# Kernel tuning notes

Hardware: AMD Instinct MI355X
Metric: run time of the kernel (lower is better)

Reference implementation:

```python
import jax, jax.numpy as jnp
import numpy as np
from jax import lax

B, R, C = 4, 64, 192          # batch, input_resolution, dim
WN, K = 16, 3                 # ka_win_num, kernel_size
WS = R // 4                   # window_size = R / sqrt(WN) = 16
DN = ('NCHW', 'OIHW', 'NCHW')


def setup_inputs() -> dict:
    key = jax.random.key(0)
    ks = jax.random.split(key, 12)
    rn = lambda k, shp, s=0.05: jax.random.normal(k, shp, dtype=jnp.float32) * s
    return {
        'x': jax.random.normal(ks[0], (B, R * R, C), dtype=jnp.float32),
        'conv1_w': rn(ks[1], (WN * C, 1, K, K), 0.1),
        'dc_w': rn(ks[2], (WN, C)),                             # grouped 1x1 (WN*C -> WN)
        'dc_b': jnp.zeros((WN,), jnp.float32),
        'l1_w': rn(ks[3], (4 * WN, WN)),
        'l1_b': jnp.zeros((4 * WN,), jnp.float32),
        'l2_w': rn(ks[4], (WN, 4 * WN)),
        'l2_b': jnp.zeros((WN,), jnp.float32),
        'gk_w': rn(ks[5], (WN,)),                               # 1x1 conv WN -> 1
        'gk_b': jnp.zeros((1,), jnp.float32),
        'fusion_w': rn(ks[6], (C, (WN + 1) * C)),               # 1x1 conv (WN+1)*C -> C
        'fusion_b': jnp.zeros((C,), jnp.float32),
    }


def _forward(x, conv1_w, dc_w, dc_b, l1_w, l1_b, l2_w, l2_b, gk_w, gk_b,
             fusion_w, fusion_b):
    # pad_feature_map is a no-op since R % WS == 0.
    xw = x.reshape(B, R // WS, WS, R // WS, WS, C)
    xw = xw.transpose(0, 1, 3, 5, 2, 4).reshape(B, WN * C, WS, WS)

    # convlayer1: depthwise conv over all WN*C channels
    y = lax.conv_general_dilated(xw, conv1_w, (1, 1), [(1, 1), (1, 1)],
                                 dimension_numbers=DN,
                                 feature_group_count=WN * C)  # (B, WN*C, WS, WS)

    # WinKernel_Reweight: pool -> grouped 1x1 -> gelu -> 1x1 -> sigmoid
    pooled = y.mean(axis=(2, 3)).reshape(B, WN, C)
    w = jnp.einsum('bwc,wc->bw', pooled, dc_w) + dc_b          # downchannel (groups=WN)
    w = jax.nn.gelu(w @ l1_w.T + l1_b, approximate=False)      # (B, 4*WN)
    w = jax.nn.sigmoid(w @ l2_w.T + l2_b)                      # (B, WN)

    kern = conv1_w.reshape(WN, C, K, K)
    kern = w[:, :, None, None, None] * kern[None]              # (B, WN, C, K, K)

    # global kernel: 1x1 conv across the WN axis
    gk = jnp.einsum('bwcij,w->bcij', kern, gk_w) + gk_b[0]     # (B, C, K, K)
    all_k = jnp.concatenate([kern, gk[:, None]], axis=1)       # (B, WN+1, C, K, K)

    # dynamic depthwise conv on the full map, per sample
    xf = x.reshape(B, R, R, C).transpose(0, 3, 1, 2)           # (B, C, R, R)
    xrep = jnp.tile(xf, (1, WN + 1, 1, 1))                     # (B, (WN+1)*C, R, R)
    kflat = all_k.reshape(B, (WN + 1) * C, 1, K, K)

    def dw(xi, ki):  # xi: ((WN+1)*C, R, R), ki: ((WN+1)*C, 1, K, K)
        return lax.conv_general_dilated(xi[None], ki, (1, 1), [(1, 1), (1, 1)],
                                        dimension_numbers=DN,
                                        feature_group_count=(WN + 1) * C)[0]

    out = jax.vmap(dw)(xrep, kflat)                            # (B, (WN+1)*C, R, R)

    # fusion 1x1 conv -> (B, C, R, R) -> (B, L, C)
    out = jnp.einsum('bdhw,cd->bhwc', out, fusion_w) + fusion_b
    return out.reshape(B, R * R, C)


def reference(x, conv1_w, dc_w, dc_b, l1_w, l1_b, l2_w, l2_b, gk_w, gk_b,
              fusion_w, fusion_b):
    return _forward(x, conv1_w, dc_w, dc_b, l1_w, l1_b, l2_w, l2_b,
                    gk_w, gk_b, fusion_w, fusion_b)
```

## Files before the change

### kernel.cpp

```cpp
#include <hip/hip_runtime.h>
#include <hip/hip_bf16.h>
#include <math.h>

#define B_  4
#define R_  64
#define C_  192
#define WN_ 16


typedef __attribute__((ext_vector_type(8))) short short8;
typedef __attribute__((ext_vector_type(4))) float floatx4;

static __device__ __forceinline__ unsigned short f2bf(float f) {
    union { float f; unsigned u; } v; v.f = f;
    unsigned r = v.u + 0x7fffu + ((v.u >> 16) & 1u);
    return (unsigned short)(r >> 16);
}

__global__ __launch_bounds__(256) void pre_kernel(
        const float* __restrict__ x,
        const float* __restrict__ conv1_w,
        const float* __restrict__ dc_w,
        float* __restrict__ w0p,
        float* __restrict__ cw_t) {
    __shared__ float part[3];
    int blk = blockIdx.x;
    int tid = threadIdx.x;

    if (blk < 256) {
        int b = blk >> 6, rest = blk & 63, win = rest >> 2, q = rest & 3;
        int wr = win >> 2, wc = win & 3;
        if (tid < 192) {
            const float* xb = x + ((size_t)b * 4096) * C_ + tid;
            float Wsum = 0.f, Rtop = 0.f, Rbot = 0.f, Cleft = 0.f, Cright = 0.f;
            float c00 = 0.f, c0F = 0.f, cF0 = 0.f, cFF = 0.f;
            #pragma unroll
            for (int pr = 0; pr < 4; ++pr) {
                int h = wr * 16 + q * 4 + pr;
                #pragma unroll
                for (int pw = 0; pw < 16; ++pw) {
                    int w = wc * 16 + pw;
                    float v = xb[(size_t)(h * 64 + w) * C_];
                    Wsum += v;
                    if (q == 0 && pr == 0) { Rtop += v; if (pw == 0) c00 = v; if (pw == 15) c0F = v; }
                    if (q == 3 && pr == 3) { Rbot += v; if (pw == 0) cF0 = v; if (pw == 15) cFF = v; }
                    if (pw == 0)  Cleft  += v;
                    if (pw == 15) Cright += v;
                }
            }
            const float* kp = conv1_w + ((size_t)(win * C_ + tid)) * 9;
            float pooled = 0.f;
            #pragma unroll
            for (int i = 0; i < 3; ++i) {
                #pragma unroll
                for (int j = 0; j < 3; ++j) {
                    int di = i - 1, dj = j - 1;
                    float S = Wsum;
                    if (di == -1) S -= Rbot;   else if (di == 1) S -= Rtop;
                    if (dj == -1) S -= Cright; else if (dj == 1) S -= Cleft;
                    if (di == -1 && dj == -1) S += cFF;
                    if (di == -1 && dj ==  1) S += cF0;
                    if (di ==  1 && dj == -1) S += c0F;
                    if (di ==  1 && dj ==  1) S += c00;
                    pooled += kp[i * 3 + j] * S;
                }
            }
            float val = (pooled * (1.f / 256.f)) * dc_w[win * C_ + tid];
            for (int off = 32; off; off >>= 1) val += __shfl_down(val, off, 64);
            if ((tid & 63) == 0) part[tid >> 6] = val;
        }
        __syncthreads();
        if (tid == 0) w0p[blk] = part[0] + part[1] + part[2];
    } else {
        int basei = (blk - 256) * 512 + tid * 2;
        #pragma unroll
        for (int e = 0; e < 2; ++e) {
            int o = basei + e;
            int t = o / 3072;
            int r = o - t * 3072;
            cw_t[o] = conv1_w[(size_t)r * 9 + t];
        }
    }
}

__global__ __launch_bounds__(192) void weff_kernel(
        const float* __restrict__ cw_t,
        const float* __restrict__ gk_w,
        const float* __restrict__ gk_b,
        const float* __restrict__ fusion_w,
        const float* __restrict__ w0p,
        const float* __restrict__ dc_b,
        const float* __restrict__ l1_w,
        const float* __restrict__ l1_b,
        const float* __restrict__ l2_w,
        const float* __restrict__ l2_b,
        unsigned short* __restrict__ Wl) {
    __shared__ float hbuf[64];
    __shared__ float s_sh[16];
    int blk = blockIdx.x;
    int b = blk / C_, co = blk % C_;
    int tid = threadIdx.x;

    if (tid < 64) {
        float a = l1_b[tid];
        #pragma unroll
        for (int w = 0; w < 16; ++w) {
            float w0 = w0p[b * 64 + w * 4 + 0] + w0p[b * 64 + w * 4 + 1]
                     + w0p[b * 64 + w * 4 + 2] + w0p[b * 64 + w * 4 + 3];
            a += (w0 + dc_b[w]) * l1_w[tid * 16 + w];
        }
        hbuf[tid] = 0.5f * a * (1.f + erff(a * 0.70710678118654752f));
    }
    __syncthreads();
    if (tid < 16) {
        float a2 = l2_b[tid];
        #pragma unroll
        for (int k = 0; k < 64; ++k) a2 += hbuf[k] * l2_w[tid * 64 + k];
        s_sh[tid] = 1.f / (1.f + expf(-a2));
    }
    __syncthreads();

    int ci = tid;
    float fg = fusion_w[(size_t)co * 3264 + 16 * C_ + ci];
    float acc[9];
    float g0 = fg * gk_b[0];
    #pragma unroll
    for (int t = 0; t < 9; ++t) acc[t] = g0;
    for (int w = 0; w < 16; ++w) {
        float coef = (fusion_w[(size_t)co * 3264 + w * C_ + ci] + fg * gk_w[w]) * s_sh[w];
        #pragma unroll
        for (int t = 0; t < 9; ++t)
            acc[t] += coef * cw_t[t * 3072 + w * C_ + ci];
    }
    #pragma unroll
    for (int t = 0; t < 9; ++t) {
        int kc = ci >> 5, cio = ci & 31;
        Wl[((((size_t)(b * 9 + t)) * 6 + kc) * C_ + co) * 32 + cio] = f2bf(acc[t]);
    }
}

__global__ __launch_bounds__(256, 1) void conv_kernel(
        const float* __restrict__ x,
        const unsigned short* __restrict__ Wl,
        const float* __restrict__ fusion_b,
        float* __restrict__ out) {
    __shared__ unsigned short Asm[3 * 3 * 66 * 32];
    const int n = blockIdx.x;
    const int g = (n & 7) * 32 + (n >> 3);
    const int b = g >> 6, h = g & 63;
    const int tid = threadIdx.x;
    const int wv = tid >> 6, lane = tid & 63;
    const int lo = lane & 15, quad = lane >> 4;
    const int n0 = wv * 48;

    const short* wp = (const short*)Wl;
    int Bbase[3];
    #pragma unroll
    for (int nt = 0; nt < 3; ++nt)
        Bbase[nt] = (b * 54 * C_ + n0 + nt * 16 + lo) * 32 + quad * 8;
    int Alds[4];
    #pragma unroll
    for (int mt = 0; mt < 4; ++mt)
        Alds[mt] = (mt * 16 + lo + 1) * 32 + quad * 8;

    floatx4 acc[4][3];
    #pragma unroll
    for (int mt = 0; mt < 4; ++mt)
        #pragma unroll
        for (int nt = 0; nt < 3; ++nt)
            acc[mt][nt] = (floatx4){0.f, 0.f, 0.f, 0.f};

    #pragma unroll
    for (int ph = 0; ph < 2; ++ph) {
        const int kc0 = ph * 3;
        #pragma unroll
        for (int r = 0; r < 3; ++r) {
            int hr = h - 1 + r;
            unsigned short* Lr = Asm + r * (3 * 66 * 32);
            if (hr >= 0 && hr < 64) {
                const float* src = x + ((size_t)(b * 4096 + hr * 64)) * C_ + kc0 * 32;
                #pragma unroll
                for (int it = 0; it < 3; ++it) {
                    int c = tid + it * 256;
                    int px = c / 12, sub = c % 12;
                    int kcl = sub >> 2, ci0 = (sub & 3) * 8;
                    const float* p = src + px * C_ + kcl * 32 + ci0;
                    float4 v0 = *(const float4*)p;
                    float4 v1 = *(const float4*)(p + 4);
                    short8 o;
                    o[0] = (short)f2bf(v0.x); o[1] = (short)f2bf(v0.y);
                    o[2] = (short)f2bf(v0.z); o[3] = (short)f2bf(v0.w);
                    o[4] = (short)f2bf(v1.x); o[5] = (short)f2bf(v1.y);
                    o[6] = (short)f2bf(v1.z); o[7] = (short)f2bf(v1.w);
                    *(short8*)(Lr + (kcl * 66 + px + 1) * 32 + ci0) = o;
                }
            } else {
                for (int c = tid; c < 792; c += 256)
                    *(short8*)(Lr + c * 8) = (short8){0, 0, 0, 0, 0, 0, 0, 0};
            }
        }
        if (tid < 72) {
            int loc = tid >> 2, j = tid & 3;
            int r = loc / 6, rem = loc % 6, kcl = rem >> 1, px = (rem & 1) * 65;
            *(short8*)(Asm + ((r * 3 + kcl) * 66 + px) * 32 + j * 8) =
                (short8){0, 0, 0, 0, 0, 0, 0, 0};
        }
        __syncthreads();

        short8 Bb[3][3], Ab[2][4];
        auto loadB = [&](int t27, int slot) {
            int tap = t27 / 3, kcl = t27 % 3;
            int s = tap * 6 + kc0 + kcl;
            #pragma unroll
            for (int nt = 0; nt < 3; ++nt)
                Bb[slot][nt] = *(const short8*)(wp + Bbase[nt] + s * (C_ * 32));
        };
        auto loadA = [&](int t27, int slot) {
            int tap = t27 / 3, kcl = t27 % 3;
            int dh = tap / 3, dw = tap % 3 - 1;
            int base = ((dh * 3 + kcl) * 66 + dw) * 32;
            #pragma unroll
            for (int mt = 0; mt < 4; ++mt)
                Ab[slot][mt] = *(const short8*)((const short*)Asm + base + Alds[mt]);
        };
        loadB(0, 0); loadB(1, 1); loadA(0, 0);
        #pragma unroll
        for (int t = 0; t < 27; ++t) {
            const int bc = t % 3, ac = t & 1;
            if (t + 2 < 27) loadB(t + 2, (t + 2) % 3);
            if (t + 1 < 27) loadA(t + 1, ac ^ 1);
            #pragma unroll
            for (int mt = 0; mt < 4; ++mt)
                #pragma unroll
                for (int nt = 0; nt < 3; ++nt)
                    acc[mt][nt] = __builtin_amdgcn_mfma_f32_16x16x32_bf16(
                        Ab[ac][mt], Bb[bc][nt], acc[mt][nt], 0, 0, 0);
        }
        __syncthreads();
    }

    #pragma unroll
    for (int nt = 0; nt < 3; ++nt) {
        const int co = n0 + nt * 16 + lo;
        const float fb = fusion_b[co];
        #pragma unroll
        for (int mt = 0; mt < 4; ++mt) {
            #pragma unroll
            for (int r = 0; r < 4; ++r) {
                const int px = mt * 16 + quad * 4 + r;
                out[((size_t)(b * 4096 + h * 64 + px)) * C_ + co] = acc[mt][nt][r] + fb;
            }
        }
    }
}

extern "C" void kernel_launch(void* const* d_in, const int* in_sizes, int n_in,
                              void* d_out, int out_size, void* d_ws, size_t ws_size,
                              hipStream_t stream) {
    const float* x        = (const float*)d_in[0];
    const float* conv1_w  = (const float*)d_in[1];
    const float* dc_w     = (const float*)d_in[2];
    const float* dc_b     = (const float*)d_in[3];
    const float* l1_w     = (const float*)d_in[4];
    const float* l1_b     = (const float*)d_in[5];
    const float* l2_w     = (const float*)d_in[6];
    const float* l2_b     = (const float*)d_in[7];
    const float* gk_w     = (const float*)d_in[8];
    const float* gk_b     = (const float*)d_in[9];
    const float* fusion_w = (const float*)d_in[10];
    const float* fusion_b = (const float*)d_in[11];
    float* out = (float*)d_out;

    char* ws = (char*)d_ws;
    float* w0p  = (float*)ws;
    float* cw_t = (float*)(ws + 1024);
    unsigned short* Wl = (unsigned short*)(ws + 1024 + 110592);

    hipLaunchKernelGGL(pre_kernel, dim3(310), dim3(256), 0, stream,
                       x, conv1_w, dc_w, w0p, cw_t);
    hipLaunchKernelGGL(weff_kernel, dim3(B_ * C_), dim3(192), 0, stream,
                       cw_t, gk_w, gk_b, fusion_w, w0p, dc_b, l1_w, l1_b, l2_w, l2_b, Wl);
    hipLaunchKernelGGL(conv_kernel, dim3(256), dim3(256), 0, stream,
                       x, Wl, fusion_b, out);
}
```

Baseline: 119.5 us.

## Pre-convert x to bf16 and stream conv tiles into LDS asynchronously

pre_kernel gets extra blocks that convert x to bf16 in a channel-chunked row layout in workspace. conv_kernel then loads its halo rows with global_load_lds straight into a double-buffered LDS region. The second phase's loads are issued before the first phase's MFMA loop, and one trailing barrier is removed. This is meant to remove the repeated fp32 reads and per-element conversions of x inside the conv kernel and to overlap loading with compute. The cost is an extra pass over x, a larger workspace and twice the LDS per block.

```diff
diff --git a/kernel.cpp b/kernel.cpp
--- a/kernel.cpp
+++ b/kernel.cpp
@@ -15,6 +15,12 @@
     union { float f; unsigned u; } v; v.f = f;
     unsigned r = v.u + 0x7fffu + ((v.u >> 16) & 1u);
     return (unsigned short)(r >> 16);
+}
+
+static __device__ __forceinline__ void gload_lds16(const void* g, void* l) {
+    __builtin_amdgcn_global_load_lds(
+        (const __attribute__((address_space(1))) unsigned*)g,
+        (__attribute__((address_space(3))) unsigned*)l, 16, 0, 0);
 }
 
 __global__ __launch_bounds__(256) void pre_kernel(
@@ -22,7 +28,8 @@
         const float* __restrict__ conv1_w,
         const float* __restrict__ dc_w,
         float* __restrict__ w0p,
-        float* __restrict__ cw_t) {
+        float* __restrict__ cw_t,
+        unsigned short* __restrict__ xbf16) {
     __shared__ float part[3];
     int blk = blockIdx.x;
     int tid = threadIdx.x;
@@ -71,7 +78,7 @@
         }
         __syncthreads();
         if (tid == 0) w0p[blk] = part[0] + part[1] + part[2];
-    } else {
+    } else if (blk < 310) {
         int basei = (blk - 256) * 512 + tid * 2;
         #pragma unroll
         for (int e = 0; e < 2; ++e) {
@@ -79,6 +86,24 @@
             int t = o / 3072;
             int r = o - t * 3072;
             cw_t[o] = conv1_w[(size_t)r * 9 + t];
+        }
+    } else {
+        int m = blk - 310;
+        int b = m >> 6, hh = m & 63;
+        const float* src = x + ((size_t)(b * 4096 + hh * 64)) * C_;
+        unsigned short* dst = xbf16 + ((size_t)(b * 64 + hh)) * 12288;
+        int px = tid >> 2, c4 = (tid & 3) * 8;
+        #pragma unroll
+        for (int j = 0; j < 6; ++j) {
+            const float* p = src + (size_t)px * C_ + j * 32 + c4;
+            float4 v0 = *(const float4*)p;
+            float4 v1 = *(const float4*)(p + 4);
+            short8 o;
+            o[0] = (short)f2bf(v0.x); o[1] = (short)f2bf(v0.y);
+            o[2] = (short)f2bf(v0.z); o[3] = (short)f2bf(v0.w);
+            o[4] = (short)f2bf(v1.x); o[5] = (short)f2bf(v1.y);
+            o[6] = (short)f2bf(v1.z); o[7] = (short)f2bf(v1.w);
+            *(short8*)(dst + j * 2048 + px * 32 + c4) = o;
         }
     }
 }
@@ -140,11 +165,11 @@
 }
 
 __global__ __launch_bounds__(256, 1) void conv_kernel(
-        const float* __restrict__ x,
+        const unsigned short* __restrict__ xbf16,
         const unsigned short* __restrict__ Wl,
         const float* __restrict__ fusion_b,
         float* __restrict__ out) {
-    __shared__ unsigned short Asm[3 * 3 * 66 * 32];
+    __shared__ unsigned short Asm[2 * 3 * 3 * 66 * 32];
     const int n = blockIdx.x;
     const int g = (n & 7) * 32 + (n >> 3);
     const int b = g >> 6, h = g & 63;
@@ -170,42 +195,36 @@
         for (int nt = 0; nt < 3; ++nt)
             acc[mt][nt] = (floatx4){0.f, 0.f, 0.f, 0.f};
 
+    for (int c = tid; c < 4752; c += 256)
+        *(short8*)(Asm + c * 8) = (short8){0, 0, 0, 0, 0, 0, 0, 0};
+    __syncthreads();
+
+    auto issue_phase = [&](int buf, int ph) {
+        const int kc0 = ph * 3;
+        #pragma unroll
+        for (int i = 0; i < 9; ++i) {
+            int c = wv * 9 + i;
+            int r = c / 12, kcl = (c % 12) >> 2, q = c & 3;
+            int hr = h - 1 + r;
+            if (hr >= 0 && hr < 64) {
+                const unsigned short* src = xbf16
+                    + ((((size_t)(b * 64 + hr)) * 6 + (kc0 + kcl)) << 11)
+                    + (q << 9) + lane * 8;
+                unsigned short* dst = Asm + buf * 19008
+                    + ((r * 3 + kcl) * 66 + 1) * 32 + q * 512;
+                gload_lds16(src, dst);
+            }
+        }
+    };
+
+    issue_phase(0, 0);
+    __syncthreads();
+    issue_phase(1, 1);
+
     #pragma unroll
     for (int ph = 0; ph < 2; ++ph) {
         const int kc0 = ph * 3;
-        #pragma unroll
-        for (int r = 0; r < 3; ++r) {
-            int hr = h - 1 + r;
-            unsigned short* Lr = Asm + r * (3 * 66 * 32);
-            if (hr >= 0 && hr < 64) {
-                const float* src = x + ((size_t)(b * 4096 + hr * 64)) * C_ + kc0 * 32;
-                #pragma unroll
-                for (int it = 0; it < 3; ++it) {
-                    int c = tid + it * 256;
-                    int px = c / 12, sub = c % 12;
-                    int kcl = sub >> 2, ci0 = (sub & 3) * 8;
-                    const float* p = src + px * C_ + kcl * 32 + ci0;
-                    float4 v0 = *(const float4*)p;
-                    float4 v1 = *(const float4*)(p + 4);
-                    short8 o;
-                    o[0] = (short)f2bf(v0.x); o[1] = (short)f2bf(v0.y);
-                    o[2] = (short)f2bf(v0.z); o[3] = (short)f2bf(v0.w);
-                    o[4] = (short)f2bf(v1.x); o[5] = (short)f2bf(v1.y);
-                    o[6] = (short)f2bf(v1.z); o[7] = (short)f2bf(v1.w);
-                    *(short8*)(Lr + (kcl * 66 + px + 1) * 32 + ci0) = o;
-                }
-            } else {
-                for (int c = tid; c < 792; c += 256)
-                    *(short8*)(Lr + c * 8) = (short8){0, 0, 0, 0, 0, 0, 0, 0};
-            }
-        }
-        if (tid < 72) {
-            int loc = tid >> 2, j = tid & 3;
-            int r = loc / 6, rem = loc % 6, kcl = rem >> 1, px = (rem & 1) * 65;
-            *(short8*)(Asm + ((r * 3 + kcl) * 66 + px) * 32 + j * 8) =
-                (short8){0, 0, 0, 0, 0, 0, 0, 0};
-        }
-        __syncthreads();
+        const unsigned short* As = Asm + ph * 19008;
 
         short8 Bb[3][3], Ab[2][4];
         auto loadB = [&](int t27, int slot) {
@@ -221,7 +240,7 @@
             int base = ((dh * 3 + kcl) * 66 + dw) * 32;
             #pragma unroll
             for (int mt = 0; mt < 4; ++mt)
-                Ab[slot][mt] = *(const short8*)((const short*)Asm + base + Alds[mt]);
+                Ab[slot][mt] = *(const short8*)((const short*)As + base + Alds[mt]);
         };
         loadB(0, 0); loadB(1, 1); loadA(0, 0);
         #pragma unroll
@@ -236,7 +255,8 @@
                     acc[mt][nt] = __builtin_amdgcn_mfma_f32_16x16x32_bf16(
                         Ab[ac][mt], Bb[bc][nt], acc[mt][nt], 0, 0, 0);
         }
-        __syncthreads();
+        if (ph == 0)
+            __syncthreads();
     }
 
     #pragma unroll
@@ -275,11 +295,12 @@
     float* w0p  = (float*)ws;
     float* cw_t = (float*)(ws + 1024);
     unsigned short* Wl = (unsigned short*)(ws + 1024 + 110592);
-
-    hipLaunchKernelGGL(pre_kernel, dim3(310), dim3(256), 0, stream,
-                       x, conv1_w, dc_w, w0p, cw_t);
+    unsigned short* xbf16 = (unsigned short*)(ws + 1024 + 110592 + 2654208);
+
+    hipLaunchKernelGGL(pre_kernel, dim3(566), dim3(256), 0, stream,
+                       x, conv1_w, dc_w, w0p, cw_t, xbf16);
     hipLaunchKernelGGL(weff_kernel, dim3(B_ * C_), dim3(192), 0, stream,
                        cw_t, gk_w, gk_b, fusion_w, w0p, dc_b, l1_w, l1_b, l2_w, l2_b, Wl);
     hipLaunchKernelGGL(conv_kernel, dim3(256), dim3(256), 0, stream,
-                       x, Wl, fusion_b, out);
-}
+                       xbf16, Wl, fusion_b, out);
+}
```

After: 120.7 us. Within noise of the previous version (+1.0%).
